# Optimization experiments

Measured on AMD Instinct MI355X. Metric: run time of the kernel, lower is better.

The kernel has to match this reference:

```python
import jax, jax.numpy as jnp
import numpy as np

N_NODES = 100000
N_EDGES = 1600000
IN_F = 128
N_HEADS = 8
HEAD_D = 8  # n_hidden // n_heads = 64 // 8
NEG_SLOPE = 0.2


def setup_inputs() -> dict:
    key = jax.random.key(0)
    k1, k2, k3, k4, k5 = jax.random.split(key, 5)
    vert = jax.random.normal(k1, (N_NODES, IN_F), dtype=jnp.float32)
    edge = jax.random.randint(k2, (2, N_EDGES), 0, N_NODES, dtype=jnp.int64)
    scale_w = 1.0 / np.sqrt(IN_F)
    W = jax.random.normal(k3, (IN_F, N_HEADS, HEAD_D), dtype=jnp.float32) * scale_w
    scale_a = 1.0 / np.sqrt(HEAD_D)
    a_src = jax.random.normal(k4, (N_HEADS, HEAD_D), dtype=jnp.float32) * scale_a
    a_dst = jax.random.normal(k5, (N_HEADS, HEAD_D), dtype=jnp.float32) * scale_a
    return {"vert": vert, "edge": edge, "W": W, "a_src": a_src, "a_dst": a_dst}


def reference(vert, edge, W, a_src, a_dst):
    # Per-head linear projection: [N, H, D]
    g = jnp.einsum('nf,fhd->nhd', vert, W)
    src, dst = edge[0], edge[1]
    # Decomposed attention logits: e_ij = LeakyReLU(a_src.g_i + a_dst.g_j)
    e_s = jnp.sum(g * a_src[None], axis=-1)  # [N, H]
    e_d = jnp.sum(g * a_dst[None], axis=-1)  # [N, H]
    scores = jax.nn.leaky_relu(e_s[src] + e_d[dst], NEG_SLOPE)  # [E, H]
    # Segment softmax over incoming edges of each destination node
    m = jax.ops.segment_max(scores, dst, num_segments=N_NODES)  # [N, H]
    m = jnp.where(jnp.isneginf(m), 0.0, m)
    ex = jnp.exp(scores - m[dst])  # [E, H]
    denom = jax.ops.segment_sum(ex, dst, num_segments=N_NODES)  # [N, H]
    alpha = ex / jnp.maximum(denom[dst], 1e-16)  # [E, H]
    # Weighted message aggregation: scatter-add alpha * g[src] into dst
    msg = alpha[:, :, None] * g[src]  # [E, H, D]
    agg = jax.ops.segment_sum(msg, dst, num_segments=N_NODES)  # [N, H, D]
    out = agg.reshape(N_NODES, N_HEADS * HEAD_D)  # concat heads
    # GAT_DE trailing ELU (dropout=0.0 -> identity)
    return jax.nn.elu(out)
```

## Files before the change

### kernel.cpp

```cpp
#include <hip/hip_runtime.h>
#include <hip/hip_bf16.h>
#include <hip/hip_fp16.h>
#include <math.h>

#define N_NODES 100000
#define N_EDGES 1600000
#define IN_F    128
#define NH      8
#define HD      8
#define HID     64
#define NEG_SLOPE 0.2f

#define BSH   5
#define BSZ   32
#define NBK   3125
#define NCB   196
#define CSTR  9216
#define BCAP  832
#define NBPJ  782
#define NPB   160
#define EPB   10000
#define GSTR  16

typedef short bf16x8 __attribute__((ext_vector_type(8)));
typedef float f32x4  __attribute__((ext_vector_type(4)));

static __device__ __forceinline__ unsigned short f2bf(float x) {
    __hip_bfloat16 h = __float2bfloat16(x);
    return *(unsigned short*)&h;
}

__global__ __launch_bounds__(256) void prep_kernel(
    const float* __restrict__ W, const float* __restrict__ a_src,
    const float* __restrict__ a_dst, unsigned short* __restrict__ Bg,
    int* __restrict__ gcnt)
{
    const int tid = threadIdx.x;
    for (int i = blockIdx.x * 256 + tid; i < NCB * GSTR; i += 16 * 256) gcnt[i] = 0;
    if (blockIdx.x != 0) return;

    __shared__ __align__(16) unsigned short bl[10240];
    for (int idx = tid; idx < 128 * 16; idx += 256) {
        const int f = idx >> 4, cq = idx & 15;
        const float4 w = *(const float4*)(W + f * 64 + cq * 4);
        const int kc = f >> 5, q = (f >> 3) & 3, j = f & 7;
        const float wf[4] = {w.x, w.y, w.z, w.w};
        #pragma unroll
        for (int i = 0; i < 4; ++i) {
            const int col = cq * 4 + i;
            bl[(col >> 4) * 2048 + kc * 512 + q * 128 + (col & 15) * 8 + j] = f2bf(wf[i]);
        }
    }
    for (int idx = tid; idx < 128 * 8; idx += 256) {
        const int f = idx >> 3, h = idx & 7;
        const float4 wa = *(const float4*)(W + f * 64 + h * 8);
        const float4 wb = *(const float4*)(W + f * 64 + h * 8 + 4);
        const float4 sa = *(const float4*)(a_src + h * 8);
        const float4 sb = *(const float4*)(a_src + h * 8 + 4);
        const float4 da = *(const float4*)(a_dst + h * 8);
        const float4 db = *(const float4*)(a_dst + h * 8 + 4);
        float esv = fmaf(wa.x, sa.x, fmaf(wa.y, sa.y, fmaf(wa.z, sa.z,
                    fmaf(wa.w, sa.w, fmaf(wb.x, sb.x, fmaf(wb.y, sb.y,
                    fmaf(wb.z, sb.z, wb.w * sb.w)))))));
        float edv = fmaf(wa.x, da.x, fmaf(wa.y, da.y, fmaf(wa.z, da.z,
                    fmaf(wa.w, da.w, fmaf(wb.x, db.x, fmaf(wb.y, db.y,
                    fmaf(wb.z, db.z, wb.w * db.w)))))));
        const int kc = f >> 5, q = (f >> 3) & 3, j = f & 7;
        bl[4 * 2048 + kc * 512 + q * 128 + h * 8 + j]       = f2bf(esv);
        bl[4 * 2048 + kc * 512 + q * 128 + (8 + h) * 8 + j] = f2bf(edv);
    }
    __syncthreads();
    for (int idx = tid; idx < 1280; idx += 256)
        ((uint4*)Bg)[idx] = ((const uint4*)bl)[idx];
}

__global__ __launch_bounds__(512) void fused_pp_kernel(
    const float* __restrict__ vert, const unsigned short* __restrict__ Bg,
    __hip_bfloat16* __restrict__ gb, float* __restrict__ es, float* __restrict__ ed,
    const int* __restrict__ edge, int* __restrict__ gcnt,
    unsigned int* __restrict__ packed)
{
    __shared__ __align__(16) char smem[28672];
    const int tid = threadIdx.x;

    if (blockIdx.x < NBPJ) {
        unsigned short* b_lds = (unsigned short*)smem;
        const int nbeg = blockIdx.x * 128;
        const int lane = tid & 63, wv = tid >> 6;
        const int mn   = lane & 15, quad = lane >> 4;

        for (int idx = tid; idx < 1280; idx += 512)
            *(uint4*)(smem + idx * 16) = ((const uint4*)Bg)[idx];

        const int row = nbeg + wv * 16 + mn;
        bf16x8 afr[4];
        #pragma unroll
        for (int kc = 0; kc < 4; ++kc) {
            float4 p = make_float4(0.f, 0.f, 0.f, 0.f);
            float4 q4 = make_float4(0.f, 0.f, 0.f, 0.f);
            if (row < N_NODES) {
                const float* rp = vert + (size_t)row * IN_F + kc * 32 + quad * 8;
                p  = *(const float4*)rp;
                q4 = *(const float4*)(rp + 4);
            }
            bf16x8 a;
            a[0] = (short)f2bf(p.x);  a[1] = (short)f2bf(p.y);
            a[2] = (short)f2bf(p.z);  a[3] = (short)f2bf(p.w);
            a[4] = (short)f2bf(q4.x); a[5] = (short)f2bf(q4.y);
            a[6] = (short)f2bf(q4.z); a[7] = (short)f2bf(q4.w);
            afr[kc] = a;
        }
        __syncthreads();

        const unsigned short* bbase = b_lds + quad * 128 + mn * 8;
        f32x4 acc[5];
        #pragma unroll
        for (int c = 0; c < 5; ++c) acc[c] = (f32x4){0.f, 0.f, 0.f, 0.f};
        #pragma unroll
        for (int kc = 0; kc < 4; ++kc) {
            #pragma unroll
            for (int c = 0; c < 5; ++c) {
                const bf16x8 bfr = *(const bf16x8*)(bbase + c * 2048 + kc * 512);
                acc[c] = __builtin_amdgcn_mfma_f32_16x16x32_bf16(afr[kc], bfr, acc[c], 0, 0, 0);
            }
        }
        __syncthreads();

        unsigned short* gl = (unsigned short*)smem + wv * 1152;
        float* lesd = (float*)(smem + 18432) + wv * 320;
        #pragma unroll
        for (int c = 0; c < 4; ++c)
            #pragma unroll
            for (int r = 0; r < 4; ++r)
                gl[(quad * 4 + r) * 72 + c * 16 + mn] = f2bf(acc[c][r]);
        {
            float* dst = (mn < 8) ? (lesd + mn) : (lesd + 160 + (mn - 8));
            #pragma unroll
            for (int r = 0; r < 4; ++r) dst[(quad * 4 + r) * 10] = acc[4][r];
        }
        __syncthreads();
        {
            const int row2 = lane >> 2, part = lane & 3;
            const int node = nbeg + wv * 16 + row2;
            if (node < N_NODES) {
                const uint4* sp = (const uint4*)(gl + row2 * 72 + part * 16);
                *(uint4*)((unsigned short*)gb + (size_t)node * HID + part * 16) = sp[0];
                *(uint4*)((unsigned short*)gb + (size_t)node * HID + part * 16 + 8) = sp[1];
            }
        }
        {
            const int nl = lane >> 2, h2 = (lane & 3) * 2;
            const int node = nbeg + wv * 16 + nl;
            if (node < N_NODES) {
                *(float2*)(es + node * NH + h2) = *(const float2*)(lesd + nl * 10 + h2);
                *(float2*)(ed + node * NH + h2) = *(const float2*)(lesd + 160 + nl * 10 + h2);
            }
        }
    } else {
        int* lh    = (int*)smem;
        int* lbase = (int*)(smem + 1024);
        const int pb = blockIdx.x - NBPJ;

        if (tid < NCB) lh[tid] = 0;
        __syncthreads();
        const int4* src4 = (const int4*)(edge + pb * EPB);
        const int4* dst4 = (const int4*)(edge + N_EDGES + pb * EPB);
        for (int t = tid; t < EPB / 4; t += 512) {
            const int4 d = dst4[t];
            atomicAdd(&lh[d.x >> 9], 1);
            atomicAdd(&lh[d.y >> 9], 1);
            atomicAdd(&lh[d.z >> 9], 1);
            atomicAdd(&lh[d.w >> 9], 1);
        }
        __syncthreads();
        if (tid < NCB) {
            const int c = lh[tid];
            lbase[tid] = c ? (tid * CSTR + atomicAdd(&gcnt[tid * GSTR], c)) : 0;
            lh[tid] = 0;
        }
        __syncthreads();
        for (int t = tid; t < EPB / 4; t += 512) {
            const int4 s = src4[t];
            const int4 d = dst4[t];
            int bk, pos;
            bk = d.x >> 9; pos = min(lbase[bk] + atomicAdd(&lh[bk], 1), NCB * CSTR - 1);
            packed[pos] = ((unsigned)s.x << 9) | (unsigned)(d.x & 511);
            bk = d.y >> 9; pos = min(lbase[bk] + atomicAdd(&lh[bk], 1), NCB * CSTR - 1);
            packed[pos] = ((unsigned)s.y << 9) | (unsigned)(d.y & 511);
            bk = d.z >> 9; pos = min(lbase[bk] + atomicAdd(&lh[bk], 1), NCB * CSTR - 1);
            packed[pos] = ((unsigned)s.z << 9) | (unsigned)(d.z & 511);
            bk = d.w >> 9; pos = min(lbase[bk] + atomicAdd(&lh[bk], 1), NCB * CSTR - 1);
            packed[pos] = ((unsigned)s.w << 9) | (unsigned)(d.w & 511);
        }
    }
}

__global__ __launch_bounds__(1024) void radixb_kernel(
    const int* __restrict__ gcnt, unsigned int* __restrict__ packed,
    int2* __restrict__ nodeinfo)
{
    __shared__ unsigned int ebuf[CSTR];
    __shared__ int fh[512], fpre[512];
    __shared__ int wsum[8];
    const int tid = threadIdx.x;
    const int cb  = blockIdx.x;
    const int cnt = min(gcnt[cb * GSTR], CSTR);
    unsigned int* in = packed + (size_t)cb * CSTR;

    if (tid < 512) fh[tid] = 0;
    __syncthreads();
    for (int i = tid; i < cnt; i += 1024) {
        const unsigned v = in[i];
        ebuf[i] = v;
        atomicAdd(&fh[v & 511], 1);
    }
    __syncthreads();
    int s = 0, v = 0;
    {
        const int lane = tid & 63, wvv = tid >> 6;
        if (tid < 512) {
            v = fh[tid];
            s = v;
            #pragma unroll
            for (int off = 1; off < 64; off <<= 1) {
                const int t = __shfl_up(s, off, 64);
                if (lane >= off) s += t;
            }
            if (lane == 63) wsum[wvv] = s;
        }
        __syncthreads();
        if (tid < 8) {
            const int w = wsum[tid];
            int e = w;
            #pragma unroll
            for (int off = 1; off < 8; off <<= 1) {
                const int t = __shfl_up(e, off, 64);
                if (tid >= off) e += t;
            }
            wsum[tid] = e - w;
        }
        __syncthreads();
        if (tid < 512) {
            const int ex = s - v + wsum[wvv];
            fpre[tid] = ex;
            fh[tid]   = ex;
        }
    }
    __syncthreads();
    for (int i = tid; i < cnt; i += 1024) {
        const unsigned vv = ebuf[i];
        const int pos = atomicAdd(&fh[vv & 511], 1);
        in[pos] = ((vv >> 9) << 7) | (vv & 31);
    }
    __syncthreads();
    if (tid < 512) {
        const int node = cb * 512 + tid;
        if (node < N_NODES)
            nodeinfo[node] = make_int2(cb * CSTR + fpre[tid], fh[tid] - fpre[tid]);
    }
}

__global__ __launch_bounds__(256) void p2agg_kernel(
    const int2* __restrict__ nodeinfo, const unsigned int* __restrict__ packed,
    const unsigned short* __restrict__ gb, const float* __restrict__ es,
    const float* __restrict__ ed, float* __restrict__ out)
{
    __shared__ unsigned int ssrt[BCAP];
    __shared__ __align__(16) unsigned short pexp[BCAP * 8];
    __shared__ int sbeg[BSZ + 1];
    __shared__ __align__(16) float led[BSZ * NH];

    const int tid  = threadIdx.x;
    const int b    = blockIdx.x;
    const int nbeg = b << BSH;
    const int ebase = nodeinfo[nbeg].x;

    if (tid < BSZ) {
        const int2 ni = nodeinfo[nbeg + tid];
        sbeg[tid] = ni.x - ebase;
        if (tid == BSZ - 1) sbeg[BSZ] = ni.x + ni.y - ebase;
    }
    for (int i = tid; i < BSZ * NH; i += 256) led[i] = ed[nbeg * NH + i];
    __syncthreads();

    const int ecnt = min(sbeg[BSZ], BCAP);

    for (int i = tid; i < ecnt; i += 256) {
        const unsigned pw = packed[ebase + i];
        ssrt[i] = pw;
        const int src = (int)(pw >> 7), dl = (int)(pw & (BSZ - 1));
        const float4 e0 = *(const float4*)(es + (size_t)src * NH);
        const float4 e1 = *(const float4*)(es + (size_t)src * NH + 4);
        const float4 l0 = *(const float4*)(led + dl * NH);
        const float4 l1 = *(const float4*)(led + dl * NH + 4);
        float s[8] = {e0.x + l0.x, e0.y + l0.y, e0.z + l0.z, e0.w + l0.w,
                      e1.x + l1.x, e1.y + l1.y, e1.z + l1.z, e1.w + l1.w};
        #pragma unroll
        for (int k = 0; k < 8; ++k)
            s[k] = __expf(fmaxf(s[k], s[k] * NEG_SLOPE));
        __half2 h01 = __floats2half2_rn(s[0], s[1]);
        __half2 h23 = __floats2half2_rn(s[2], s[3]);
        __half2 h45 = __floats2half2_rn(s[4], s[5]);
        __half2 h67 = __floats2half2_rn(s[6], s[7]);
        uint4 w;
        w.x = *(unsigned*)&h01; w.y = *(unsigned*)&h23;
        w.z = *(unsigned*)&h45; w.w = *(unsigned*)&h67;
        *(uint4*)(pexp + i * 8) = w;
    }
    __syncthreads();

    const int lane = tid & 63;
    const int wv   = tid >> 6;
    const int c4   = lane & 15;
    const int eg   = lane >> 4;
    const int h    = c4 >> 1;
    const unsigned c4_8 = (unsigned)(c4 << 3);
    const char* gbase = (const char*)gb;

    for (int n = wv; n < BSZ; n += 4) {
        const int end = min(sbeg[n + 1], ecnt);
        const int beg = min(sbeg[n], end);
        float l = 0.f, a0 = 0.f, a1 = 0.f, a2 = 0.f, a3 = 0.f;
        int i = beg;
        for (; i + 16 <= end; i += 16) {
            const unsigned pw0 = ssrt[i + eg];
            const unsigned pw1 = ssrt[i + 4 + eg];
            const unsigned pw2 = ssrt[i + 8 + eg];
            const unsigned pw3 = ssrt[i + 12 + eg];
            const uint2 g0 = *(const uint2*)(gbase + ((pw0 & ~127u) | c4_8));
            const uint2 g1 = *(const uint2*)(gbase + ((pw1 & ~127u) | c4_8));
            const uint2 g2 = *(const uint2*)(gbase + ((pw2 & ~127u) | c4_8));
            const uint2 g3 = *(const uint2*)(gbase + ((pw3 & ~127u) | c4_8));
            const float pe0 = __half2float(*(const __half*)(pexp + ((i + eg) << 3) + h));
            const float pe1 = __half2float(*(const __half*)(pexp + ((i + 4 + eg) << 3) + h));
            const float pe2 = __half2float(*(const __half*)(pexp + ((i + 8 + eg) << 3) + h));
            const float pe3 = __half2float(*(const __half*)(pexp + ((i + 12 + eg) << 3) + h));
            a0 = fmaf(pe0, __uint_as_float(g0.x << 16), a0);
            a1 = fmaf(pe0, __uint_as_float(g0.x & 0xFFFF0000u), a1);
            a2 = fmaf(pe0, __uint_as_float(g0.y << 16), a2);
            a3 = fmaf(pe0, __uint_as_float(g0.y & 0xFFFF0000u), a3);
            a0 = fmaf(pe1, __uint_as_float(g1.x << 16), a0);
            a1 = fmaf(pe1, __uint_as_float(g1.x & 0xFFFF0000u), a1);
            a2 = fmaf(pe1, __uint_as_float(g1.y << 16), a2);
            a3 = fmaf(pe1, __uint_as_float(g1.y & 0xFFFF0000u), a3);
            a0 = fmaf(pe2, __uint_as_float(g2.x << 16), a0);
            a1 = fmaf(pe2, __uint_as_float(g2.x & 0xFFFF0000u), a1);
            a2 = fmaf(pe2, __uint_as_float(g2.y << 16), a2);
            a3 = fmaf(pe2, __uint_as_float(g2.y & 0xFFFF0000u), a3);
            a0 = fmaf(pe3, __uint_as_float(g3.x << 16), a0);
            a1 = fmaf(pe3, __uint_as_float(g3.x & 0xFFFF0000u), a1);
            a2 = fmaf(pe3, __uint_as_float(g3.y << 16), a2);
            a3 = fmaf(pe3, __uint_as_float(g3.y & 0xFFFF0000u), a3);
            l += (pe0 + pe1) + (pe2 + pe3);
        }
        if (i < end) {
            const int e0 = i + eg, e1 = i + 4 + eg, e2 = i + 8 + eg, e3 = i + 12 + eg;
            const int ec0 = min(e0, end - 1), ec1 = min(e1, end - 1);
            const int ec2 = min(e2, end - 1), ec3 = min(e3, end - 1);
            const unsigned pw0 = ssrt[ec0];
            const unsigned pw1 = ssrt[ec1];
            const unsigned pw2 = ssrt[ec2];
            const unsigned pw3 = ssrt[ec3];
            const uint2 g0 = *(const uint2*)(gbase + ((pw0 & ~127u) | c4_8));
            const uint2 g1 = *(const uint2*)(gbase + ((pw1 & ~127u) | c4_8));
            const uint2 g2 = *(const uint2*)(gbase + ((pw2 & ~127u) | c4_8));
            const uint2 g3 = *(const uint2*)(gbase + ((pw3 & ~127u) | c4_8));
            float pe0 = __half2float(*(const __half*)(pexp + (ec0 << 3) + h));
            float pe1 = __half2float(*(const __half*)(pexp + (ec1 << 3) + h));
            float pe2 = __half2float(*(const __half*)(pexp + (ec2 << 3) + h));
            float pe3 = __half2float(*(const __half*)(pexp + (ec3 << 3) + h));
            pe0 = (e0 < end) ? pe0 : 0.f;
            pe1 = (e1 < end) ? pe1 : 0.f;
            pe2 = (e2 < end) ? pe2 : 0.f;
            pe3 = (e3 < end) ? pe3 : 0.f;
            a0 = fmaf(pe0, __uint_as_float(g0.x << 16), a0);
            a1 = fmaf(pe0, __uint_as_float(g0.x & 0xFFFF0000u), a1);
            a2 = fmaf(pe0, __uint_as_float(g0.y << 16), a2);
            a3 = fmaf(pe0, __uint_as_float(g0.y & 0xFFFF0000u), a3);
            a0 = fmaf(pe1, __uint_as_float(g1.x << 16), a0);
            a1 = fmaf(pe1, __uint_as_float(g1.x & 0xFFFF0000u), a1);
            a2 = fmaf(pe1, __uint_as_float(g1.y << 16), a2);
            a3 = fmaf(pe1, __uint_as_float(g1.y & 0xFFFF0000u), a3);
            a0 = fmaf(pe2, __uint_as_float(g2.x << 16), a0);
            a1 = fmaf(pe2, __uint_as_float(g2.x & 0xFFFF0000u), a1);
            a2 = fmaf(pe2, __uint_as_float(g2.y << 16), a2);
            a3 = fmaf(pe2, __uint_as_float(g2.y & 0xFFFF0000u), a3);
            a0 = fmaf(pe3, __uint_as_float(g3.x << 16), a0);
            a1 = fmaf(pe3, __uint_as_float(g3.x & 0xFFFF0000u), a1);
            a2 = fmaf(pe3, __uint_as_float(g3.y << 16), a2);
            a3 = fmaf(pe3, __uint_as_float(g3.y & 0xFFFF0000u), a3);
            l += (pe0 + pe1) + (pe2 + pe3);
        }
        l  += __shfl_xor(l, 16);  l  += __shfl_xor(l, 32);
        a0 += __shfl_xor(a0, 16); a0 += __shfl_xor(a0, 32);
        a1 += __shfl_xor(a1, 16); a1 += __shfl_xor(a1, 32);
        a2 += __shfl_xor(a2, 16); a2 += __shfl_xor(a2, 32);
        a3 += __shfl_xor(a3, 16); a3 += __shfl_xor(a3, 32);
        if (eg == 0) {
            const float rl = 1.f / fmaxf(l, 1e-16f);
            float o0 = a0 * rl, o1 = a1 * rl, o2 = a2 * rl, o3 = a3 * rl;
            o0 = (o0 > 0.f) ? o0 : (__expf(o0) - 1.f);
            o1 = (o1 > 0.f) ? o1 : (__expf(o1) - 1.f);
            o2 = (o2 > 0.f) ? o2 : (__expf(o2) - 1.f);
            o3 = (o3 > 0.f) ? o3 : (__expf(o3) - 1.f);
            *(float4*)(out + (size_t)(nbeg + n) * HID + c4 * 4) =
                make_float4(o0, o1, o2, o3);
        }
    }
}

extern "C" void kernel_launch(void* const* d_in, const int* in_sizes, int n_in,
                              void* d_out, int out_size, void* d_ws, size_t ws_size,
                              hipStream_t stream)
{
    const float* vert  = (const float*)d_in[0];
    const int*   edge  = (const int*)  d_in[1];
    const float* W     = (const float*)d_in[2];
    const float* a_src = (const float*)d_in[3];
    const float* a_dst = (const float*)d_in[4];
    float* out = (float*)d_out;

    char* ws = (char*)d_ws;
    __hip_bfloat16* gb     = (__hip_bfloat16*)(ws);
    float*          es     = (float*)(ws + 12800000);
    float*          ed     = (float*)(ws + 16000000);
    unsigned int*   packed = (unsigned int*)(ws + 19200000);
    int*            gcnt   = (int*)(ws + 26425344);
    int2*           nodeinfo = (int2*)(ws + 26437888);
    unsigned short* Bg     = (unsigned short*)(ws + 27237888);

    prep_kernel<<<16, 256, 0, stream>>>(W, a_src, a_dst, Bg, gcnt);
    fused_pp_kernel<<<NBPJ + NPB, 512, 0, stream>>>(
        vert, Bg, gb, es, ed, edge, gcnt, packed);
    radixb_kernel<<<NCB, 1024, 0, stream>>>(gcnt, packed, nodeinfo);
    p2agg_kernel<<<NBK, 256, 0, stream>>>(nodeinfo, packed, (const unsigned short*)gb, es, ed, out);
}
```

Measured before the change: 176.3 us.

## Stage edge partition through shared memory for coalesced writes with finer buckets

The edge-partition phase now buffers 2000-edge chunks in shared memory, sorts them locally by coarse bucket with a block prefix scan, and writes each bucket's run contiguously to global memory instead of scattering individual 4-byte stores. Buckets shrink from 512 to 256 destination nodes (392 buckets), which lowers per-bucket capacity and the fine histogram size in the radix kernel. That kernel also sorts into a shared buffer and copies back coalesced instead of scattering in place. The cost is more barriers and scans per chunk, plus larger shared-memory use that can reduce occupancy.

```diff
diff --git a/kernel.cpp b/kernel.cpp
--- a/kernel.cpp
+++ b/kernel.cpp
@@ -14,12 +14,13 @@
 #define BSH   5
 #define BSZ   32
 #define NBK   3125
-#define NCB   196
-#define CSTR  9216
+#define NCB   392
+#define CSTR  4800
 #define BCAP  832
 #define NBPJ  782
 #define NPB   160
 #define EPB   10000
+#define CCH   2000
 #define GSTR  16
 
 typedef short bf16x8 __attribute__((ext_vector_type(8)));
@@ -158,39 +159,95 @@
         }
     } else {
         int* lh    = (int*)smem;
-        int* lbase = (int*)(smem + 1024);
+        int* lbase = (int*)(smem + 1600);
+        int* lcur  = (int*)(smem + 3200);
+        int* cpre  = (int*)(smem + 4800);
+        int* wsum8 = (int*)(smem + 6400);
+        unsigned* ebuf = (unsigned*)(smem + 6464);
+        unsigned short* bkb = (unsigned short*)(smem + 14464);
+        unsigned* sbuf = (unsigned*)(smem + 18464);
         const int pb = blockIdx.x - NBPJ;
-
-        if (tid < NCB) lh[tid] = 0;
-        __syncthreads();
         const int4* src4 = (const int4*)(edge + pb * EPB);
         const int4* dst4 = (const int4*)(edge + N_EDGES + pb * EPB);
+        const int lane = tid & 63, w8 = tid >> 6;
+
+        if (tid < NCB) lh[tid] = 0;
+        __syncthreads();
         for (int t = tid; t < EPB / 4; t += 512) {
             const int4 d = dst4[t];
-            atomicAdd(&lh[d.x >> 9], 1);
-            atomicAdd(&lh[d.y >> 9], 1);
-            atomicAdd(&lh[d.z >> 9], 1);
-            atomicAdd(&lh[d.w >> 9], 1);
+            atomicAdd(&lh[d.x >> 8], 1);
+            atomicAdd(&lh[d.y >> 8], 1);
+            atomicAdd(&lh[d.z >> 8], 1);
+            atomicAdd(&lh[d.w >> 8], 1);
         }
         __syncthreads();
         if (tid < NCB) {
             const int c = lh[tid];
-            lbase[tid] = c ? (tid * CSTR + atomicAdd(&gcnt[tid * GSTR], c)) : 0;
-            lh[tid] = 0;
-        }
-        __syncthreads();
-        for (int t = tid; t < EPB / 4; t += 512) {
-            const int4 s = src4[t];
-            const int4 d = dst4[t];
-            int bk, pos;
-            bk = d.x >> 9; pos = min(lbase[bk] + atomicAdd(&lh[bk], 1), NCB * CSTR - 1);
-            packed[pos] = ((unsigned)s.x << 9) | (unsigned)(d.x & 511);
-            bk = d.y >> 9; pos = min(lbase[bk] + atomicAdd(&lh[bk], 1), NCB * CSTR - 1);
-            packed[pos] = ((unsigned)s.y << 9) | (unsigned)(d.y & 511);
-            bk = d.z >> 9; pos = min(lbase[bk] + atomicAdd(&lh[bk], 1), NCB * CSTR - 1);
-            packed[pos] = ((unsigned)s.z << 9) | (unsigned)(d.z & 511);
-            bk = d.w >> 9; pos = min(lbase[bk] + atomicAdd(&lh[bk], 1), NCB * CSTR - 1);
-            packed[pos] = ((unsigned)s.w << 9) | (unsigned)(d.w & 511);
+            int r = c ? atomicAdd(&gcnt[tid * GSTR], c) : 0;
+            r = min(r, max(CSTR - c, 0));
+            lbase[tid] = tid * CSTR + r;
+            lcur[tid] = 0;
+        }
+        __syncthreads();
+        for (int c0 = 0; c0 < EPB / 4; c0 += CCH / 4) {
+            if (tid < NCB) lh[tid] = 0;
+            __syncthreads();
+            for (int t = c0 + tid; t < c0 + CCH / 4; t += 512) {
+                const int4 s = src4[t];
+                const int4 d = dst4[t];
+                const int base = (t - c0) * 4;
+                int bk;
+                bk = d.x >> 8; ebuf[base]     = ((unsigned)s.x << 8) | (d.x & 255);
+                bkb[base]     = (unsigned short)bk; atomicAdd(&lh[bk], 1);
+                bk = d.y >> 8; ebuf[base + 1] = ((unsigned)s.y << 8) | (d.y & 255);
+                bkb[base + 1] = (unsigned short)bk; atomicAdd(&lh[bk], 1);
+                bk = d.z >> 8; ebuf[base + 2] = ((unsigned)s.z << 8) | (d.z & 255);
+                bkb[base + 2] = (unsigned short)bk; atomicAdd(&lh[bk], 1);
+                bk = d.w >> 8; ebuf[base + 3] = ((unsigned)s.w << 8) | (d.w & 255);
+                bkb[base + 3] = (unsigned short)bk; atomicAdd(&lh[bk], 1);
+            }
+            __syncthreads();
+            {
+                int v = (tid < NCB) ? lh[tid] : 0;
+                int s = v;
+                #pragma unroll
+                for (int off = 1; off < 64; off <<= 1) {
+                    const int t2 = __shfl_up(s, off, 64);
+                    if (lane >= off) s += t2;
+                }
+                if (lane == 63) wsum8[w8] = s;
+                __syncthreads();
+                if (tid < 8) {
+                    const int w0 = wsum8[tid];
+                    int e = w0;
+                    #pragma unroll
+                    for (int off = 1; off < 8; off <<= 1) {
+                        const int t2 = __shfl_up(e, off, 64);
+                        if (tid >= off) e += t2;
+                    }
+                    wsum8[tid] = e - w0;
+                }
+                __syncthreads();
+                const int ex = s - v + wsum8[w8];
+                if (tid < NCB) { cpre[tid] = ex; lh[tid] = ex; }
+                if (tid == 0) cpre[NCB] = CCH;
+            }
+            __syncthreads();
+            for (int i = tid; i < CCH; i += 512) {
+                const int bk = (int)bkb[i];
+                const int pos = atomicAdd(&lh[bk], 1);
+                sbuf[pos] = ebuf[i];
+            }
+            __syncthreads();
+            for (int bk = w8; bk < NCB; bk += 8) {
+                const int sb = cpre[bk];
+                const int len = cpre[bk + 1] - sb;
+                unsigned* dst = packed + lbase[bk] + lcur[bk];
+                for (int j = lane; j < len; j += 64) dst[j] = sbuf[sb + j];
+            }
+            __syncthreads();
+            if (tid < NCB) lcur[tid] += cpre[tid + 1] - cpre[tid];
+            __syncthreads();
         }
     }
 }
@@ -200,25 +257,26 @@
     int2* __restrict__ nodeinfo)
 {
     __shared__ unsigned int ebuf[CSTR];
-    __shared__ int fh[512], fpre[512];
-    __shared__ int wsum[8];
+    __shared__ unsigned int sbuf[CSTR];
+    __shared__ int fh[256], fpre[256];
+    __shared__ int wsum[4];
     const int tid = threadIdx.x;
     const int cb  = blockIdx.x;
     const int cnt = min(gcnt[cb * GSTR], CSTR);
     unsigned int* in = packed + (size_t)cb * CSTR;
 
-    if (tid < 512) fh[tid] = 0;
+    if (tid < 256) fh[tid] = 0;
     __syncthreads();
     for (int i = tid; i < cnt; i += 1024) {
         const unsigned v = in[i];
         ebuf[i] = v;
-        atomicAdd(&fh[v & 511], 1);
+        atomicAdd(&fh[v & 255], 1);
     }
     __syncthreads();
     int s = 0, v = 0;
     {
         const int lane = tid & 63, wvv = tid >> 6;
-        if (tid < 512) {
+        if (tid < 256) {
             v = fh[tid];
             s = v;
             #pragma unroll
@@ -229,18 +287,18 @@
             if (lane == 63) wsum[wvv] = s;
         }
         __syncthreads();
-        if (tid < 8) {
+        if (tid < 4) {
             const int w = wsum[tid];
             int e = w;
             #pragma unroll
-            for (int off = 1; off < 8; off <<= 1) {
+            for (int off = 1; off < 4; off <<= 1) {
                 const int t = __shfl_up(e, off, 64);
                 if (tid >= off) e += t;
             }
             wsum[tid] = e - w;
         }
         __syncthreads();
-        if (tid < 512) {
+        if (tid < 256) {
             const int ex = s - v + wsum[wvv];
             fpre[tid] = ex;
             fh[tid]   = ex;
@@ -249,12 +307,13 @@
     __syncthreads();
     for (int i = tid; i < cnt; i += 1024) {
         const unsigned vv = ebuf[i];
-        const int pos = atomicAdd(&fh[vv & 511], 1);
-        in[pos] = ((vv >> 9) << 7) | (vv & 31);
-    }
-    __syncthreads();
-    if (tid < 512) {
-        const int node = cb * 512 + tid;
+        const int pos = atomicAdd(&fh[vv & 255], 1);
+        sbuf[pos] = ((vv >> 8) << 7) | (vv & 31);
+    }
+    __syncthreads();
+    for (int i = tid; i < cnt; i += 1024) in[i] = sbuf[i];
+    if (tid < 256) {
+        const int node = cb * 256 + tid;
         if (node < N_NODES)
             nodeinfo[node] = make_int2(cb * CSTR + fpre[tid], fh[tid] - fpre[tid]);
     }
@@ -425,9 +484,9 @@
     float*          es     = (float*)(ws + 12800000);
     float*          ed     = (float*)(ws + 16000000);
     unsigned int*   packed = (unsigned int*)(ws + 19200000);
-    int*            gcnt   = (int*)(ws + 26425344);
-    int2*           nodeinfo = (int2*)(ws + 26437888);
-    unsigned short* Bg     = (unsigned short*)(ws + 27237888);
+    int*            gcnt   = (int*)(ws + 26726400);
+    int2*           nodeinfo = (int2*)(ws + 26751488);
+    unsigned short* Bg     = (unsigned short*)(ws + 27551488);
 
     prep_kernel<<<16, 256, 0, stream>>>(W, a_src, a_dst, Bg, gcnt);
     fused_pp_kernel<<<NBPJ + NPB, 512, 0, stream>>>(
```

Result: slower. 215.5 us (+22.2%).
